# Kernel tuning notes

Measured on AMD Instinct MI355X. Metric: run time of the kernel, lower is better.

Reference implementation:

```python
import jax, jax.numpy as jnp
import numpy as np

T, B, F = 512, 512, 14
H1, H2 = 32, 64


def setup_inputs() -> dict:
    key = jax.random.key(0)
    ks = jax.random.split(key, 16)
    s1 = 1.0 / np.sqrt(H1)
    s2 = 1.0 / np.sqrt(H2)
    u = lambda k, shape, s: jax.random.uniform(k, shape, jnp.float32, -s, s)
    return {
        "x": jax.random.normal(ks[0], (T, B, F), jnp.float32),
        # LSTM layer 1 (PyTorch gate order i,f,g,o)
        "W_ih1": u(ks[1], (4 * H1, F), s1),
        "W_hh1": u(ks[2], (4 * H1, H1), s1),
        "b_ih1": u(ks[3], (4 * H1,), s1),
        "b_hh1": u(ks[4], (4 * H1,), s1),
        # LSTM layer 2
        "W_ih2": u(ks[5], (4 * H2, H1), s2),
        "W_hh2": u(ks[6], (4 * H2, H2), s2),
        "b_ih2": u(ks[7], (4 * H2,), s2),
        "b_hh2": u(ks[8], (4 * H2,), s2),
        # MLP head
        "W_fc1": u(ks[9], (8, H2), 1.0 / np.sqrt(H2)),
        "b_fc1": u(ks[10], (8,), 1.0 / np.sqrt(H2)),
        "W_fc2": u(ks[11], (8, 8), 1.0 / np.sqrt(8)),
        "b_fc2": u(ks[12], (8,), 1.0 / np.sqrt(8)),
        "W_fc": u(ks[13], (1, 8), 1.0 / np.sqrt(8)),
        "b_fc": u(ks[14], (1,), 1.0 / np.sqrt(8)),
    }


def _gates(g, c):
    # PyTorch LSTM gate order: input, forget, cell(g), output
    i, f, gg, o = jnp.split(g, 4, axis=-1)
    c_new = jax.nn.sigmoid(f) * c + jax.nn.sigmoid(i) * jnp.tanh(gg)
    h_new = jax.nn.sigmoid(o) * jnp.tanh(c_new)
    return h_new, c_new


def reference(x, W_ih1, W_hh1, b_ih1, b_hh1, W_ih2, W_hh2, b_ih2, b_hh2,
              W_fc1, b_fc1, W_fc2, b_fc2, W_fc, b_fc):
    Bv = x.shape[1]
    # Fold the input projection of layer 1 outside the scan (one big GEMM).
    xg = jnp.einsum('tbf,gf->tbg', x, W_ih1) + b_ih1 + b_hh1  # [T,B,4H1]

    def step(carry, xg_t):
        h1, c1, h2 = carry
        h1, c1 = _gates(xg_t + h1 @ W_hh1.T, c1)
        # Layer 2: original code never carries c_t2 -> incoming cell is always 0.
        g2 = h1 @ W_ih2.T + b_ih2 + h2 @ W_hh2.T + b_hh2
        h2, _ = _gates(g2, jnp.zeros((Bv, H2), x.dtype))
        return (h1, c1, h2), None

    init = (jnp.zeros((Bv, H1), x.dtype),
            jnp.zeros((Bv, H1), x.dtype),
            jnp.zeros((Bv, H2), x.dtype))
    (h1, c1, h2), _ = jax.lax.scan(step, init, xg)

    out = jax.nn.relu(h2)
    out = jax.nn.relu(out @ W_fc1.T + b_fc1)
    out = jax.nn.relu(out @ W_fc2.T + b_fc2)
    return out @ W_fc.T + b_fc  # [B,1]
```

## Files before the change

kernel.cpp:

```cpp
#include <hip/hip_runtime.h>
#include <math.h>

#define TT 512
#define BB 512
#define FF 14
#define H1 32
#define H2 64
#define NR 8
#define NBLK (BB / NR)

typedef _Float16 half8   __attribute__((ext_vector_type(8)));
typedef _Float16 half4_t __attribute__((ext_vector_type(4)));
typedef float    float4v __attribute__((ext_vector_type(4)));

typedef __attribute__((address_space(1))) const half4_t g_half4;

#if __has_builtin(__builtin_amdgcn_exp2f)
__device__ __forceinline__ float exp2_(float x) { return __builtin_amdgcn_exp2f(x); }
#else
__device__ __forceinline__ float exp2_(float x) { return exp2f(x); }
#endif
__device__ __forceinline__ float rcpf_(float x) { return __builtin_amdgcn_rcpf(x); }

__device__ __forceinline__ float dpp_ror8_(float v) {
    return __int_as_float(__builtin_amdgcn_update_dpp(
        0, __float_as_int(v), 0x128 , 0xF, 0xF, true));
}

#define K1L 1.4426950408889634f
#define K2L 2.8853901617779268f

__device__ __forceinline__ float4v mfma16(half8 a, half8 b, float4v c) {
    return __builtin_amdgcn_mfma_f32_16x16x32_f16(a, b, c, 0, 0, 0);
}

__device__ __forceinline__ int bfrag_off(int k, int n) {
    const int slab = k >> 5, k5 = k & 31;
    const int dl = n + 16 * ((k5 >> 3) & 3);
    const int dw = (k5 >> 1) & 3;
    return ((slab * 256 + dl * 4 + dw) << 1) | (k5 & 1);
}

__global__ __launch_bounds__(512)
void xg_precompute(const float* __restrict__ x,
                   const float* __restrict__ Wih1,
                   const float* __restrict__ bih1,
                   const float* __restrict__ bhh1,
                   _Float16* __restrict__ xg)
{
    const int t    = blockIdx.x >> 3;
    const int seg  = blockIdx.x & 7;
    const int l    = threadIdx.x;
    const int lane = l & 63;
    const int w    = l >> 6;
    const int n    = lane & 15;
    const int quad = lane >> 4;
    const int u1   = w * 4 + quad;

    __shared__ __align__(16) float xs[64 * FF];

    {
        const float* src = x + ((size_t)t * BB + seg * 64) * FF;
        if (l < 448) {
            const float2 v = ((const float2*)src)[l];
            ((float2*)xs)[l] = v;
        }
    }

    float wr[4][FF];
    float bs[4];
    #pragma unroll
    for (int r = 0; r < 4; ++r) {
        const int row = r * 32 + u1;
        #pragma unroll
        for (int f = 0; f < FF; ++f) wr[r][f] = Wih1[row * FF + f];
        bs[r] = bih1[row] + bhh1[row];
    }
    __syncthreads();

    half4_t* og = (half4_t*)xg + (size_t)t * (NBLK * 256);
    #pragma unroll 2
    for (int bi = 0; bi < 8; ++bi) {
        const int blk = seg * 8 + bi;
        const int rb  = (bi * 8 + (n & 7)) * FF;
        float xv[FF];
        #pragma unroll
        for (int e = 0; e < 7; ++e) {
            const float2 v = *(const float2*)&xs[rb + 2 * e];
            xv[2 * e] = v.x; xv[2 * e + 1] = v.y;
        }
        half4_t o16;
        #pragma unroll
        for (int r = 0; r < 4; ++r) {
            float a = bs[r];
            #pragma unroll
            for (int f = 0; f < FF; ++f) a = fmaf(xv[f], wr[r][f], a);
            o16[r] = (_Float16)a;
        }
        if (n < 8) og[blk * 256 + u1 * 8 + n] = o16;
    }
}

#define XGOFF(t_) ((size_t)(t_) * (NBLK * 256))

__global__ __launch_bounds__(768)
__attribute__((amdgpu_waves_per_eu(3, 3)))
void lstm3_v23(
    const _Float16* __restrict__ xg,
    const float* __restrict__ Wih2, const float* __restrict__ Whh1,
    const float* __restrict__ Whh2,
    const float* __restrict__ bih2, const float* __restrict__ bhh2,
    const float* __restrict__ Wfc1, const float* __restrict__ bfc1,
    const float* __restrict__ Wfc2, const float* __restrict__ bfc2,
    const float* __restrict__ Wfc,  const float* __restrict__ bfc,
    float* __restrict__ out)
{
    const int row0 = blockIdx.x * NR;
    const int l    = threadIdx.x;
    const int lane = l & 63;
    const int wv   = l >> 6;
    const bool isL1 = (wv < 4);
    const int w2   = wv - 4;
    const int n    = lane & 15;
    const int quad = lane >> 4;
    const int hi   = n >> 3;

    __shared__ __align__(16) unsigned s2f[2][3 * 256];
    __shared__ _Float16 h2plain[NR][H2];
    __shared__ float mlp1[NR][8];
    __shared__ float mlp2[NR][8];

    half8 a2[2][3];
    float4v bias2[2];
    if (!isL1) {
        #pragma unroll
        for (int tt = 0; tt < 2; ++tt) {
            const int T = 2 * w2 + tt;
            const int m = T * 16 + n;
            const int row = (m & 3) * 64 + (m >> 2);
            #pragma unroll
            for (int s = 0; s < 3; ++s) {
                const int k0 = s * 32 + quad * 8;
                half8 a;
                if (k0 < H1) {
                    #pragma unroll
                    for (int j = 0; j < 8; ++j) a[j] = (_Float16)Wih2[row * H1 + k0 + j];
                } else {
                    #pragma unroll
                    for (int j = 0; j < 8; ++j) a[j] = (_Float16)Whh2[row * H2 + (k0 - H1) + j];
                }
                a2[tt][s] = a;
            }
            const int u = T * 4 + quad;
            #pragma unroll
            for (int r = 0; r < 4; ++r) {
                const int br = r * 64 + u;
                bias2[tt][r] = bih2[br] + bhh2[br];
            }
        }
    }

    half8 a1h0, a1h1;
    if (isL1) {
        #pragma unroll
        for (int tt = 0; tt < 2; ++tt) {
            const int m = (2 * wv + tt) * 16 + n;
            const int row = (m & 3) * 32 + (m >> 2);
            half8 a;
            #pragma unroll
            for (int j = 0; j < 8; ++j)
                a[j] = (_Float16)Whh1[row * H1 + quad * 8 + j];
            if (tt == 0) a1h0 = a; else a1h1 = a;
        }
    }

    const int u1sel = (2 * wv + hi) * 4 + quad;
    const int offB  = bfrag_off(u1sel & 31, n & 7);
    const int u2sel = (2 * w2 + hi) * 4 + quad;
    const int off2n = bfrag_off(32 + (u2sel & 63), n & 7);

    const g_half4* xgb = (const g_half4*)((const half4_t*)xg
                        + (size_t)blockIdx.x * 256 + ((u1sel & 31) * 8 + (n & 7)));

    float c1r = 0.0f;

    for (int z = l; z < 2 * 3 * 256; z += 768) ((unsigned*)s2f)[z] = 0u;

    half4_t xg0 = {0,0,0,0}, xgA = {0,0,0,0}, xgB = {0,0,0,0},
            xgC = {0,0,0,0}, xgD = {0,0,0,0};
    if (isL1) {
        xg0 = xgb[XGOFF(0)];
        xgA = xgb[XGOFF(1)];
        xgB = xgb[XGOFF(2)];
        xgC = xgb[XGOFF(3)];
        xgD = xgb[XGOFF(4)];
    }
    __syncthreads();

#define LSTM_STEP(i_, CP_, RP_, XG_) do {                                          \
        if (isL1) {                                                                \
            const half8 tb0 = *(const half8*)(s2f[RP_] + lane * 4);                \
            const half4_t xh = XG_;                                                \
            { int tn_ = (i_) + 4; if (tn_ > TT - 1) tn_ = TT - 1;                  \
              XG_ = xgb[XGOFF(tn_)]; }                                             \
            const float4v z4 = {0.0f, 0.0f, 0.0f, 0.0f};                           \
            float4v p0 = mfma16(a1h0, tb0, z4);                                    \
            float4v p1 = mfma16(a1h1, tb0, z4);                                    \
            float4v ps;                                                            \
            _Pragma("unroll")                                                      \
            for (int r = 0; r < 4; ++r) {                                          \
                const float sw = dpp_ror8_(p1[r]);                                 \
                ps[r] = hi ? sw : p0[r];                                           \
            }                                                                      \
            const float g0 = ps[0] + (float)xh[0];                                 \
            const float g1 = ps[1] + (float)xh[1];                                 \
            const float g2 = ps[2] + (float)xh[2];                                 \
            const float g3 = ps[3] + (float)xh[3];                                 \
            const float Ei = exp2_(-K1L * g0);                                     \
            const float Ef = exp2_(-K1L * g1);                                     \
            const float Eg = exp2_(-K2L * g2);                                     \
            const float Eo = exp2_(-K1L * g3);                                     \
            const float P  = (1.0f + Ei) * (1.0f + Eg);                            \
            const float pf = 1.0f + Ef;                                            \
            const float cn = fmaf(c1r, P, pf * (1.0f - Eg)) * rcpf_(pf * P);       \
            c1r = cn;                                                              \
            const float Ec = exp2_(-K2L * cn);                                     \
            const float hh = (1.0f - Ec) * rcpf_((1.0f + Eo) * (1.0f + Ec));       \
            ((_Float16*)s2f[CP_])[offB] = (_Float16)hh;                            \
        } else {                                                                   \
            const half8 tb0 = *(const half8*)(s2f[RP_] + lane * 4);                \
            const half8 tb1 = *(const half8*)(s2f[RP_] + 256 + lane * 4);          \
            const half8 tb2 = *(const half8*)(s2f[RP_] + 512 + lane * 4);          \
            float4v p0 = bias2[0];                                                 \
            p0 = mfma16(a2[0][0], tb0, p0);                                        \
            p0 = mfma16(a2[0][1], tb1, p0);                                        \
            p0 = mfma16(a2[0][2], tb2, p0);                                        \
            float4v p1 = bias2[1];                                                 \
            p1 = mfma16(a2[1][0], tb0, p1);                                        \
            p1 = mfma16(a2[1][1], tb1, p1);                                        \
            p1 = mfma16(a2[1][2], tb2, p1);                                        \
            float4v ps;                                                            \
            _Pragma("unroll")                                                      \
            for (int r = 0; r < 4; ++r) {                                          \
                const float sw = dpp_ror8_(p1[r]);                                 \
                ps[r] = hi ? sw : p0[r];                                           \
            }                                                                      \
            const float Ei = exp2_(-K1L * ps[0]);                                  \
            const float Eg = exp2_(-K2L * ps[2]);                                  \
            const float Eo = exp2_(-K1L * ps[3]);                                  \
            const float c2 = (1.0f - Eg) * rcpf_((1.0f + Ei) * (1.0f + Eg));       \
            const float Ec = exp2_(-K2L * c2);                                     \
            const float h  = (1.0f - Ec) * rcpf_((1.0f + Eo) * (1.0f + Ec));       \
            ((_Float16*)s2f[CP_])[off2n] = (_Float16)h;                            \
        }                                                                          \
        asm volatile("s_waitcnt lgkmcnt(0)" ::: "memory");                         \
        __builtin_amdgcn_s_barrier();                                              \
        asm volatile("" ::: "memory");                                             \
    } while (0)

    {
        if (isL1) {
            const float gi = (float)xg0[0], gg = (float)xg0[2], go = (float)xg0[3];
            const float Ei = exp2_(-K1L * gi);
            const float Eg = exp2_(-K2L * gg);
            const float Eo = exp2_(-K1L * go);
            const float cn = (1.0f - Eg) * rcpf_((1.0f + Ei) * (1.0f + Eg));
            c1r = cn;
            const float Ec = exp2_(-K2L * cn);
            const float hh = (1.0f - Ec) * rcpf_((1.0f + Eo) * (1.0f + Ec));
            ((_Float16*)s2f[0])[offB] = (_Float16)hh;
        }
        asm volatile("s_waitcnt lgkmcnt(0)" ::: "memory");
        __builtin_amdgcn_s_barrier();
        asm volatile("" ::: "memory");
    }

    #pragma unroll 1
    for (int ii = 0; ii < 127; ++ii) {
        const int i0 = 4 * ii + 1;
        LSTM_STEP(i0,     1, 0, xgA);
        LSTM_STEP(i0 + 1, 0, 1, xgB);
        LSTM_STEP(i0 + 2, 1, 0, xgC);
        LSTM_STEP(i0 + 3, 0, 1, xgD);
    }
    LSTM_STEP(509, 1, 0, xgA);
    LSTM_STEP(510, 0, 1, xgB);
    LSTM_STEP(511, 1, 0, xgC);

    if (!isL1) {
        const half8 tb0 = *(const half8*)(s2f[1] + lane * 4);
        const half8 tb1 = *(const half8*)(s2f[1] + 256 + lane * 4);
        const half8 tb2 = *(const half8*)(s2f[1] + 512 + lane * 4);
        float4v p0 = bias2[0];
        p0 = mfma16(a2[0][0], tb0, p0);
        p0 = mfma16(a2[0][1], tb1, p0);
        p0 = mfma16(a2[0][2], tb2, p0);
        float4v p1 = bias2[1];
        p1 = mfma16(a2[1][0], tb0, p1);
        p1 = mfma16(a2[1][1], tb1, p1);
        p1 = mfma16(a2[1][2], tb2, p1);
        float4v ps;
        #pragma unroll
        for (int r = 0; r < 4; ++r) {
            const float sw = dpp_ror8_(p1[r]);
            ps[r] = hi ? sw : p0[r];
        }
        const float Ei = exp2_(-K1L * ps[0]);
        const float Eg = exp2_(-K2L * ps[2]);
        const float Eo = exp2_(-K1L * ps[3]);
        const float c2 = (1.0f - Eg) * rcpf_((1.0f + Ei) * (1.0f + Eg));
        const float Ec = exp2_(-K2L * c2);
        const float h  = (1.0f - Ec) * rcpf_((1.0f + Eo) * (1.0f + Ec));
        h2plain[n & 7][u2sel] = (_Float16)h;
    }
    __syncthreads();

    if (l < NR * 8) {
        const int rr = l >> 3, j = l & 7;
        float a = bfc1[j];
        #pragma unroll
        for (int k = 0; k < H2; ++k)
            a = fmaf(fmaxf((float)h2plain[rr][k], 0.0f), Wfc1[j * H2 + k], a);
        mlp1[rr][j] = fmaxf(a, 0.0f);
    }
    __syncthreads();
    if (l < NR * 8) {
        const int rr = l >> 3, j = l & 7;
        float a = bfc2[j];
        #pragma unroll
        for (int k = 0; k < 8; ++k) a = fmaf(mlp1[rr][k], Wfc2[j * 8 + k], a);
        mlp2[rr][j] = fmaxf(a, 0.0f);
    }
    __syncthreads();
    if (l < NR) {
        float a = bfc[0];
        #pragma unroll
        for (int k = 0; k < 8; ++k) a = fmaf(mlp2[l][k], Wfc[k], a);
        out[row0 + l] = a;
    }
#undef LSTM_STEP
}

__device__ __forceinline__ float sigmoidf_(float x) { return rcpf_(1.0f + __expf(-x)); }
__device__ __forceinline__ float tanhf_(float x) {
    float e = __expf(-2.0f * fabsf(x));
    float t = (1.0f - e) * rcpf_(1.0f + e);
    return copysignf(t, x);
}

__global__ __launch_bounds__(512)
__attribute__((amdgpu_waves_per_eu(2, 2)))
void lstm3_kernel(
    const float* __restrict__ x,
    const float* __restrict__ Wih1, const float* __restrict__ Whh1,
    const float* __restrict__ bih1, const float* __restrict__ bhh1,
    const float* __restrict__ Wih2, const float* __restrict__ Whh2,
    const float* __restrict__ bih2, const float* __restrict__ bhh2,
    const float* __restrict__ Wfc1, const float* __restrict__ bfc1,
    const float* __restrict__ Wfc2, const float* __restrict__ bfc2,
    const float* __restrict__ Wfc,  const float* __restrict__ bfc,
    float* __restrict__ out)
{
    const int row0 = blockIdx.x * 16;
    const int l    = threadIdx.x;
    const int lane = l & 63;
    const int w    = l >> 6;
    const int n    = lane & 15;
    const int quad = lane >> 4;

    __shared__ __align__(16) unsigned s2f[2][3 * 256];
    __shared__ _Float16 h2plain[16][H2];
    __shared__ float mlp1[16][8];
    __shared__ float mlp2[16][8];

    half8 a2[2][3];
    float4v bias2[2];
    #pragma unroll
    for (int tt = 0; tt < 2; ++tt) {
        const int T = 2 * w + tt;
        const int m = T * 16 + n;
        const int row = (m & 3) * 64 + (m >> 2);
        #pragma unroll
        for (int s = 0; s < 3; ++s) {
            const int k0 = s * 32 + quad * 8;
            half8 a;
            if (k0 < H1) {
                #pragma unroll
                for (int j = 0; j < 8; ++j) a[j] = (_Float16)Wih2[row * H1 + k0 + j];
            } else {
                #pragma unroll
                for (int j = 0; j < 8; ++j) a[j] = (_Float16)Whh2[row * H2 + (k0 - H1) + j];
            }
            a2[tt][s] = a;
        }
        const int u = T * 4 + quad;
        #pragma unroll
        for (int r = 0; r < 4; ++r) {
            const int br = r * 64 + u;
            bias2[tt][r] = bih2[br] + bhh2[br];
        }
    }

    half8 a1x, a1h;
    float4v bias1;
    {
        const int m = w * 16 + n;
        const int row = (m & 3) * 32 + (m >> 2);
        #pragma unroll
        for (int j = 0; j < 8; ++j) {
            const int k = quad * 8 + j;
            a1x[j] = (_Float16)((k < FF) ? Wih1[row * FF + k] : 0.0f);
            a1h[j] = (_Float16)Whh1[row * H1 + k];
        }
        const int u1_ = w * 4 + quad;
        #pragma unroll
        for (int r = 0; r < 4; ++r) {
            const int br = r * 32 + u1_;
            bias1[r] = bih1[br] + bhh1[br];
        }
    }

    const int u1   = w * 4 + quad;
    const int offB = bfrag_off(u1, n);
    int off2[2];
    #pragma unroll
    for (int tt = 0; tt < 2; ++tt)
        off2[tt] = bfrag_off(32 + (2 * w + tt) * 4 + quad, n);

    const int b1q  = quad & 1;
    const int xrow = (row0 + n) * FF;
    const int xo0 = 8 * b1q;
    const int xo1 = 8 * b1q + 2;
    const int xo2 = 8 * b1q + 4;
    const int xo3 = 6 * b1q + 6;

    float c1r = 0.0f;
    float2 xr0[4], xr1[4];

    for (int z = l; z < 2 * 3 * 256; z += 512) ((unsigned*)s2f)[z] = 0u;

    {
        const float* xp = x + xrow;
        xr0[0] = *(const float2*)(xp + xo0);
        xr0[1] = *(const float2*)(xp + xo1);
        xr0[2] = *(const float2*)(xp + xo2);
        xr0[3] = *(const float2*)(xp + xo3);
        const float* xq = x + BB * FF + xrow;
        xr1[0] = *(const float2*)(xq + xo0);
        xr1[1] = *(const float2*)(xq + xo1);
        xr1[2] = *(const float2*)(xq + xo2);
        xr1[3] = *(const float2*)(xq + xo3);
    }
    __syncthreads();

#define LSTM_STEP_F(i_, CP_, RP_, XR_) do {                                        \
        const half8 tb0 = *(const half8*)(s2f[RP_] + lane * 4);                    \
        const half8 tb1 = *(const half8*)(s2f[RP_] + 256 + lane * 4);              \
        const half8 tb2 = *(const half8*)(s2f[RP_] + 512 + lane * 4);              \
        half8 xb;                                                                  \
        xb[0] = (_Float16)XR_[0].x; xb[1] = (_Float16)XR_[0].y;                    \
        xb[2] = (_Float16)XR_[1].x; xb[3] = (_Float16)XR_[1].y;                    \
        xb[4] = (_Float16)XR_[2].x; xb[5] = (_Float16)XR_[2].y;                    \
        xb[6] = (_Float16)XR_[3].x; xb[7] = (_Float16)XR_[3].y;                    \
        { int tn_ = (i_) + 2; if (tn_ > TT - 1) tn_ = TT - 1;                      \
          const float* xp_ = x + tn_ * (BB * FF) + xrow;                           \
          XR_[0] = *(const float2*)(xp_ + xo0);                                    \
          XR_[1] = *(const float2*)(xp_ + xo1);                                    \
          XR_[2] = *(const float2*)(xp_ + xo2);                                    \
          XR_[3] = *(const float2*)(xp_ + xo3); }                                  \
        float4v acc1 = mfma16(a1x, xb, bias1);                                     \
        acc1 = mfma16(a1h, tb0, acc1);                                             \
        const float cn1 = sigmoidf_(acc1[1]) * c1r                                 \
                        + sigmoidf_(acc1[0]) * tanhf_(acc1[2]);                    \
        c1r = cn1;                                                                 \
        ((_Float16*)s2f[CP_])[offB] = (_Float16)(sigmoidf_(acc1[3]) * tanhf_(cn1));\
        _Pragma("unroll")                                                          \
        for (int tt = 0; tt < 2; ++tt) {                                           \
            float4v acc = bias2[tt];                                               \
            acc = mfma16(a2[tt][0], tb0, acc);                                     \
            acc = mfma16(a2[tt][1], tb1, acc);                                     \
            acc = mfma16(a2[tt][2], tb2, acc);                                     \
            const float cn = sigmoidf_(acc[0]) * tanhf_(acc[2]);                   \
            const float h  = sigmoidf_(acc[3]) * tanhf_(cn);                       \
            ((_Float16*)s2f[CP_])[off2[tt]] = (_Float16)h;                         \
        }                                                                          \
        asm volatile("s_waitcnt lgkmcnt(0)" ::: "memory");                         \
        __builtin_amdgcn_s_barrier();                                              \
        asm volatile("" ::: "memory");                                             \
    } while (0)

    {
        half8 xb;
        xb[0] = (_Float16)xr0[0].x; xb[1] = (_Float16)xr0[0].y;
        xb[2] = (_Float16)xr0[1].x; xb[3] = (_Float16)xr0[1].y;
        xb[4] = (_Float16)xr0[2].x; xb[5] = (_Float16)xr0[2].y;
        xb[6] = (_Float16)xr0[3].x; xb[7] = (_Float16)xr0[3].y;
        {   const float* xp_ = x + 2 * (BB * FF) + xrow;
            xr0[0] = *(const float2*)(xp_ + xo0);
            xr0[1] = *(const float2*)(xp_ + xo1);
            xr0[2] = *(const float2*)(xp_ + xo2);
            xr0[3] = *(const float2*)(xp_ + xo3); }
        float4v acc1 = mfma16(a1x, xb, bias1);
        const float cn1 = sigmoidf_(acc1[0]) * tanhf_(acc1[2]);
        c1r = cn1;
        ((_Float16*)s2f[0])[offB] = (_Float16)(sigmoidf_(acc1[3]) * tanhf_(cn1));
        asm volatile("s_waitcnt lgkmcnt(0)" ::: "memory");
        __builtin_amdgcn_s_barrier();
        asm volatile("" ::: "memory");
    }

    #pragma unroll 1
    for (int ii = 0; ii < 255; ++ii) {
        const int i0 = 2 * ii + 1;
        LSTM_STEP_F(i0,     1, 0, xr1);
        LSTM_STEP_F(i0 + 1, 0, 1, xr0);
    }
    LSTM_STEP_F(511, 1, 0, xr1);

    {
        const half8 tb0 = *(const half8*)(s2f[1] + lane * 4);
        const half8 tb1 = *(const half8*)(s2f[1] + 256 + lane * 4);
        const half8 tb2 = *(const half8*)(s2f[1] + 512 + lane * 4);
        #pragma unroll
        for (int tt = 0; tt < 2; ++tt) {
            float4v acc = bias2[tt];
            acc = mfma16(a2[tt][0], tb0, acc);
            acc = mfma16(a2[tt][1], tb1, acc);
            acc = mfma16(a2[tt][2], tb2, acc);
            const float cn = sigmoidf_(acc[0]) * tanhf_(acc[2]);
            const float h  = sigmoidf_(acc[3]) * tanhf_(cn);
            h2plain[n][(2 * w + tt) * 4 + quad] = (_Float16)h;
        }
        __syncthreads();
    }

    if (l < 16 * 8) {
        const int rr = l >> 3, j = l & 7;
        float a = bfc1[j];
        #pragma unroll
        for (int k = 0; k < H2; ++k)
            a = fmaf(fmaxf((float)h2plain[rr][k], 0.0f), Wfc1[j * H2 + k], a);
        mlp1[rr][j] = fmaxf(a, 0.0f);
    }
    __syncthreads();
    if (l < 16 * 8) {
        const int rr = l >> 3, j = l & 7;
        float a = bfc2[j];
        #pragma unroll
        for (int k = 0; k < 8; ++k) a = fmaf(mlp1[rr][k], Wfc2[j * 8 + k], a);
        mlp2[rr][j] = fmaxf(a, 0.0f);
    }
    __syncthreads();
    if (l < 16) {
        float a = bfc[0];
        #pragma unroll
        for (int k = 0; k < 8; ++k) a = fmaf(mlp2[l][k], Wfc[k], a);
        out[row0 + l] = a;
    }
#undef LSTM_STEP_F
}

extern "C" void kernel_launch(void* const* d_in, const int* in_sizes, int n_in,
                              void* d_out, int out_size, void* d_ws, size_t ws_size,
                              hipStream_t stream) {
    const float* x    = (const float*)d_in[0];
    const float* Wih1 = (const float*)d_in[1];
    const float* Whh1 = (const float*)d_in[2];
    const float* bih1 = (const float*)d_in[3];
    const float* bhh1 = (const float*)d_in[4];
    const float* Wih2 = (const float*)d_in[5];
    const float* Whh2 = (const float*)d_in[6];
    const float* bih2 = (const float*)d_in[7];
    const float* bhh2 = (const float*)d_in[8];
    const float* Wfc1 = (const float*)d_in[9];
    const float* bfc1 = (const float*)d_in[10];
    const float* Wfc2 = (const float*)d_in[11];
    const float* bfc2 = (const float*)d_in[12];
    const float* Wfc  = (const float*)d_in[13];
    const float* bfc  = (const float*)d_in[14];
    float* out = (float*)d_out;

    const size_t xg_bytes = (size_t)TT * NBLK * 256 * sizeof(half4_t);
    if (d_ws != nullptr && ws_size >= xg_bytes) {
        _Float16* xg = (_Float16*)d_ws;
        xg_precompute<<<dim3(TT * 8), dim3(512), 0, stream>>>(x, Wih1, bih1, bhh1, xg);
        lstm3_v23<<<dim3(NBLK), dim3(768), 0, stream>>>(
            xg, Wih2, Whh1, Whh2, bih2, bhh2,
            Wfc1, bfc1, Wfc2, bfc2, Wfc, bfc, out);
    } else {
        lstm3_kernel<<<dim3(BB / 16), dim3(512), 0, stream>>>(
            x, Wih1, Whh1, bih1, bhh1, Wih2, Whh2, bih2, bhh2,
            Wfc1, bfc1, Wfc2, bfc2, Wfc, bfc, out);
    }
}
```

Before: 297.8 us.

## Halve batch rows per block and widen per-wave MFMA tiles in LSTM recurrence

Each block of the recurrent kernel now handles 4 batch rows instead of 8, which doubles the block count to 128. Each block runs 6 waves instead of 12, and each wave computes four MFMA gate tiles instead of two. The tile results are combined with three DPP row rotations and a 4-way select. The xg layout keeps 64 super-blocks, and each block indexes its half through blockIdx parity. The aim is to spread the latency-bound recurrence over more CUs with fewer waves per block, at the cost of more MFMAs per wave on the serial critical path and MFMA columns that are only half used.

```diff
diff --git a/kernel.cpp b/kernel.cpp
--- a/kernel.cpp
+++ b/kernel.cpp
@@ -6,8 +6,9 @@
 #define FF 14
 #define H1 32
 #define H2 64
-#define NR 8
+#define NR 4
 #define NBLK (BB / NR)
+#define XSB 64
 
 typedef _Float16 half8   __attribute__((ext_vector_type(8)));
 typedef _Float16 half4_t __attribute__((ext_vector_type(4)));
@@ -22,9 +23,17 @@
 #endif
 __device__ __forceinline__ float rcpf_(float x) { return __builtin_amdgcn_rcpf(x); }
 
+__device__ __forceinline__ float dpp_ror4_(float v) {
+    return __int_as_float(__builtin_amdgcn_update_dpp(
+        0, __float_as_int(v), 0x124, 0xF, 0xF, true));
+}
 __device__ __forceinline__ float dpp_ror8_(float v) {
     return __int_as_float(__builtin_amdgcn_update_dpp(
-        0, __float_as_int(v), 0x128 , 0xF, 0xF, true));
+        0, __float_as_int(v), 0x128, 0xF, 0xF, true));
+}
+__device__ __forceinline__ float dpp_ror12_(float v) {
+    return __int_as_float(__builtin_amdgcn_update_dpp(
+        0, __float_as_int(v), 0x12C, 0xF, 0xF, true));
 }
 
 #define K1L 1.4426950408889634f
@@ -78,10 +87,10 @@
     }
     __syncthreads();
 
-    half4_t* og = (half4_t*)xg + (size_t)t * (NBLK * 256);
+    half4_t* og = (half4_t*)xg + (size_t)t * (XSB * 256);
     #pragma unroll 2
     for (int bi = 0; bi < 8; ++bi) {
-        const int blk = seg * 8 + bi;
+        const int sb  = seg * 8 + bi;
         const int rb  = (bi * 8 + (n & 7)) * FF;
         float xv[FF];
         #pragma unroll
@@ -97,15 +106,15 @@
             for (int f = 0; f < FF; ++f) a = fmaf(xv[f], wr[r][f], a);
             o16[r] = (_Float16)a;
         }
-        if (n < 8) og[blk * 256 + u1 * 8 + n] = o16;
-    }
-}
-
-#define XGOFF(t_) ((size_t)(t_) * (NBLK * 256))
-
-__global__ __launch_bounds__(768)
-__attribute__((amdgpu_waves_per_eu(3, 3)))
-void lstm3_v23(
+        if (n < 8) og[sb * 256 + u1 * 8 + n] = o16;
+    }
+}
+
+#define XGOFF(t_) ((size_t)(t_) * (XSB * 256))
+
+__global__ __launch_bounds__(384)
+__attribute__((amdgpu_waves_per_eu(2, 2)))
+void lstm3_v24(
     const _Float16* __restrict__ xg,
     const float* __restrict__ Wih2, const float* __restrict__ Whh1,
     const float* __restrict__ Whh2,
@@ -119,23 +128,24 @@
     const int l    = threadIdx.x;
     const int lane = l & 63;
     const int wv   = l >> 6;
-    const bool isL1 = (wv < 4);
-    const int w2   = wv - 4;
+    const bool isL1 = (wv < 2);
+    const int w2   = wv - 2;
     const int n    = lane & 15;
     const int quad = lane >> 4;
-    const int hi   = n >> 3;
+    const int sq   = n >> 2;
+    const int cc   = n & 3;
 
     __shared__ __align__(16) unsigned s2f[2][3 * 256];
     __shared__ _Float16 h2plain[NR][H2];
     __shared__ float mlp1[NR][8];
     __shared__ float mlp2[NR][8];
 
-    half8 a2[2][3];
-    float4v bias2[2];
+    half8 a2[4][3];
+    float4v bias2[4];
     if (!isL1) {
         #pragma unroll
-        for (int tt = 0; tt < 2; ++tt) {
-            const int T = 2 * w2 + tt;
+        for (int tt = 0; tt < 4; ++tt) {
+            const int T = 4 * w2 + tt;
             const int m = T * 16 + n;
             const int row = (m & 3) * 64 + (m >> 2);
             #pragma unroll
@@ -160,31 +170,35 @@
         }
     }
 
-    half8 a1h0, a1h1;
+    half8 a1h0, a1h1, a1h2, a1h3;
     if (isL1) {
         #pragma unroll
-        for (int tt = 0; tt < 2; ++tt) {
-            const int m = (2 * wv + tt) * 16 + n;
+        for (int tt = 0; tt < 4; ++tt) {
+            const int m = (4 * wv + tt) * 16 + n;
             const int row = (m & 3) * 32 + (m >> 2);
             half8 a;
             #pragma unroll
             for (int j = 0; j < 8; ++j)
                 a[j] = (_Float16)Whh1[row * H1 + quad * 8 + j];
-            if (tt == 0) a1h0 = a; else a1h1 = a;
-        }
-    }
-
-    const int u1sel = (2 * wv + hi) * 4 + quad;
-    const int offB  = bfrag_off(u1sel & 31, n & 7);
-    const int u2sel = (2 * w2 + hi) * 4 + quad;
-    const int off2n = bfrag_off(32 + (u2sel & 63), n & 7);
+            if      (tt == 0) a1h0 = a;
+            else if (tt == 1) a1h1 = a;
+            else if (tt == 2) a1h2 = a;
+            else              a1h3 = a;
+        }
+    }
+
+    const int u1sel = (4 * wv + sq) * 4 + quad;
+    const int offB  = bfrag_off(u1sel & 31, cc);
+    const int u2sel = (4 * w2 + sq) * 4 + quad;
+    const int off2n = bfrag_off(32 + (u2sel & 63), cc);
 
     const g_half4* xgb = (const g_half4*)((const half4_t*)xg
-                        + (size_t)blockIdx.x * 256 + ((u1sel & 31) * 8 + (n & 7)));
+            + (size_t)(blockIdx.x >> 1) * 256
+            + ((u1sel & 31) * 8 + (blockIdx.x & 1) * 4 + cc));
 
     float c1r = 0.0f;
 
-    for (int z = l; z < 2 * 3 * 256; z += 768) ((unsigned*)s2f)[z] = 0u;
+    for (int z = l; z < 2 * 3 * 256; z += 384) ((unsigned*)s2f)[z] = 0u;
 
     half4_t xg0 = {0,0,0,0}, xgA = {0,0,0,0}, xgB = {0,0,0,0},
             xgC = {0,0,0,0}, xgD = {0,0,0,0};
@@ -196,6 +210,18 @@
         xgD = xgb[XGOFF(4)];
     }
     __syncthreads();
+
+#define MERGE4(PS_, P0_, P1_, P2_, P3_) do {                                       \
+        _Pragma("unroll")                                                          \
+        for (int r = 0; r < 4; ++r) {                                              \
+            const float q1 = dpp_ror12_(P1_[r]);                                   \
+            const float q2 = dpp_ror8_(P2_[r]);                                    \
+            const float q3 = dpp_ror4_(P3_[r]);                                    \
+            const float t01 = (sq == 1) ? q1 : P0_[r];                             \
+            const float t23 = (sq == 3) ? q3 : q2;                                 \
+            PS_[r] = (sq >= 2) ? t23 : t01;                                        \
+        }                                                                          \
+    } while (0)
 
 #define LSTM_STEP(i_, CP_, RP_, XG_) do {                                          \
         if (isL1) {                                                                \
@@ -206,12 +232,10 @@
             const float4v z4 = {0.0f, 0.0f, 0.0f, 0.0f};                           \
             float4v p0 = mfma16(a1h0, tb0, z4);                                    \
             float4v p1 = mfma16(a1h1, tb0, z4);                                    \
+            float4v p2 = mfma16(a1h2, tb0, z4);                                    \
+            float4v p3 = mfma16(a1h3, tb0, z4);                                    \
             float4v ps;                                                            \
-            _Pragma("unroll")                                                      \
-            for (int r = 0; r < 4; ++r) {                                          \
-                const float sw = dpp_ror8_(p1[r]);                                 \
-                ps[r] = hi ? sw : p0[r];                                           \
-            }                                                                      \
+            MERGE4(ps, p0, p1, p2, p3);                                            \
             const float g0 = ps[0] + (float)xh[0];                                 \
             const float g1 = ps[1] + (float)xh[1];                                 \
             const float g2 = ps[2] + (float)xh[2];                                 \
@@ -239,12 +263,16 @@
             p1 = mfma16(a2[1][0], tb0, p1);                                        \
             p1 = mfma16(a2[1][1], tb1, p1);                                        \
             p1 = mfma16(a2[1][2], tb2, p1);                                        \
+            float4v p2 = bias2[2];                                                 \
+            p2 = mfma16(a2[2][0], tb0, p2);                                        \
+            p2 = mfma16(a2[2][1], tb1, p2);                                        \
+            p2 = mfma16(a2[2][2], tb2, p2);                                        \
+            float4v p3 = bias2[3];                                                 \
+            p3 = mfma16(a2[3][0], tb0, p3);                                        \
+            p3 = mfma16(a2[3][1], tb1, p3);                                        \
+            p3 = mfma16(a2[3][2], tb2, p3);                                        \
             float4v ps;                                                            \
-            _Pragma("unroll")                                                      \
-            for (int r = 0; r < 4; ++r) {                                          \
-                const float sw = dpp_ror8_(p1[r]);                                 \
-                ps[r] = hi ? sw : p0[r];                                           \
-            }                                                                      \
+            MERGE4(ps, p0, p1, p2, p3);                                            \
             const float Ei = exp2_(-K1L * ps[0]);                                  \
             const float Eg = exp2_(-K2L * ps[2]);                                  \
             const float Eo = exp2_(-K1L * ps[3]);                                  \
@@ -299,19 +327,23 @@
         p1 = mfma16(a2[1][0], tb0, p1);
         p1 = mfma16(a2[1][1], tb1, p1);
         p1 = mfma16(a2[1][2], tb2, p1);
+        float4v p2 = bias2[2];
+        p2 = mfma16(a2[2][0], tb0, p2);
+        p2 = mfma16(a2[2][1], tb1, p2);
+        p2 = mfma16(a2[2][2], tb2, p2);
+        float4v p3 = bias2[3];
+        p3 = mfma16(a2[3][0], tb0, p3);
+        p3 = mfma16(a2[3][1], tb1, p3);
+        p3 = mfma16(a2[3][2], tb2, p3);
         float4v ps;
-        #pragma unroll
-        for (int r = 0; r < 4; ++r) {
-            const float sw = dpp_ror8_(p1[r]);
-            ps[r] = hi ? sw : p0[r];
-        }
+        MERGE4(ps, p0, p1, p2, p3);
         const float Ei = exp2_(-K1L * ps[0]);
         const float Eg = exp2_(-K2L * ps[2]);
         const float Eo = exp2_(-K1L * ps[3]);
         const float c2 = (1.0f - Eg) * rcpf_((1.0f + Ei) * (1.0f + Eg));
         const float Ec = exp2_(-K2L * c2);
         const float h  = (1.0f - Ec) * rcpf_((1.0f + Eo) * (1.0f + Ec));
-        h2plain[n & 7][u2sel] = (_Float16)h;
+        h2plain[cc][u2sel] = (_Float16)h;
     }
     __syncthreads();
 
@@ -339,6 +371,7 @@
         out[row0 + l] = a;
     }
 #undef LSTM_STEP
+#undef MERGE4
 }
 
 __device__ __forceinline__ float sigmoidf_(float x) { return rcpf_(1.0f + __expf(-x)); }
@@ -580,11 +613,11 @@
     const float* bfc  = (const float*)d_in[14];
     float* out = (float*)d_out;
 
-    const size_t xg_bytes = (size_t)TT * NBLK * 256 * sizeof(half4_t);
+    const size_t xg_bytes = (size_t)TT * XSB * 256 * sizeof(half4_t);
     if (d_ws != nullptr && ws_size >= xg_bytes) {
         _Float16* xg = (_Float16*)d_ws;
         xg_precompute<<<dim3(TT * 8), dim3(512), 0, stream>>>(x, Wih1, bih1, bhh1, xg);
-        lstm3_v23<<<dim3(NBLK), dim3(768), 0, stream>>>(
+        lstm3_v24<<<dim3(NBLK), dim3(384), 0, stream>>>(
             xg, Wih2, Whh1, Whh2, bih2, bhh2,
             Wfc1, bfc1, Wfc2, bfc2, Wfc, bfc, out);
     } else {
```

Measured after the change: 298.1 us. About the same (+0.1%).

## Interleave two independent 8-row batch groups per LSTM block

Applied to the files above, without the earlier changes.

Each recurrent block now carries two independent 8-row batch groups, A and B. Each group has its own shared-memory h buffers, cell-state registers and xg prefetch registers. The MFMA and activation work of the two groups is interleaved inside every time step, so the two dependency chains can hide each other's latency. This halves the grid to 32 blocks and lengthens each step's instruction stream, and it shares one barrier per step between both groups. The xg workspace is re-indexed by 8-row sub-block so the precompute kernel stays unchanged.

```diff
diff --git a/kernel.cpp b/kernel.cpp
--- a/kernel.cpp
+++ b/kernel.cpp
@@ -6,8 +6,10 @@
 #define FF 14
 #define H1 32
 #define H2 64
-#define NR 8
+#define NRG 8
+#define NR 16
 #define NBLK (BB / NR)
+#define XSB 64
 
 typedef _Float16 half8   __attribute__((ext_vector_type(8)));
 typedef _Float16 half4_t __attribute__((ext_vector_type(4)));
@@ -78,10 +80,10 @@
     }
     __syncthreads();
 
-    half4_t* og = (half4_t*)xg + (size_t)t * (NBLK * 256);
+    half4_t* og = (half4_t*)xg + (size_t)t * (XSB * 256);
     #pragma unroll 2
     for (int bi = 0; bi < 8; ++bi) {
-        const int blk = seg * 8 + bi;
+        const int sb  = seg * 8 + bi;
         const int rb  = (bi * 8 + (n & 7)) * FF;
         float xv[FF];
         #pragma unroll
@@ -97,15 +99,15 @@
             for (int f = 0; f < FF; ++f) a = fmaf(xv[f], wr[r][f], a);
             o16[r] = (_Float16)a;
         }
-        if (n < 8) og[blk * 256 + u1 * 8 + n] = o16;
-    }
-}
-
-#define XGOFF(t_) ((size_t)(t_) * (NBLK * 256))
+        if (n < 8) og[sb * 256 + u1 * 8 + n] = o16;
+    }
+}
+
+#define XGOFF(t_) ((size_t)(t_) * (XSB * 256))
 
 __global__ __launch_bounds__(768)
 __attribute__((amdgpu_waves_per_eu(3, 3)))
-void lstm3_v23(
+void lstm3_v26(
     const _Float16* __restrict__ xg,
     const float* __restrict__ Wih2, const float* __restrict__ Whh1,
     const float* __restrict__ Whh2,
@@ -125,7 +127,8 @@
     const int quad = lane >> 4;
     const int hi   = n >> 3;
 
-    __shared__ __align__(16) unsigned s2f[2][3 * 256];
+    __shared__ __align__(16) unsigned s2fA[2][3 * 256];
+    __shared__ __align__(16) unsigned s2fB[2][3 * 256];
     __shared__ _Float16 h2plain[NR][H2];
     __shared__ float mlp1[NR][8];
     __shared__ float mlp2[NR][8];
@@ -179,79 +182,108 @@
     const int u2sel = (2 * w2 + hi) * 4 + quad;
     const int off2n = bfrag_off(32 + (u2sel & 63), n & 7);
 
-    const g_half4* xgb = (const g_half4*)((const half4_t*)xg
-                        + (size_t)blockIdx.x * 256 + ((u1sel & 31) * 8 + (n & 7)));
-
-    float c1r = 0.0f;
-
-    for (int z = l; z < 2 * 3 * 256; z += 768) ((unsigned*)s2f)[z] = 0u;
-
-    half4_t xg0 = {0,0,0,0}, xgA = {0,0,0,0}, xgB = {0,0,0,0},
-            xgC = {0,0,0,0}, xgD = {0,0,0,0};
+    const int xge = (u1sel & 31) * 8 + (n & 7);
+    const g_half4* xgbA = (const g_half4*)((const half4_t*)xg
+                        + (size_t)(2 * blockIdx.x)     * 256 + xge);
+    const g_half4* xgbB = (const g_half4*)((const half4_t*)xg
+                        + (size_t)(2 * blockIdx.x + 1) * 256 + xge);
+
+    float c1rA = 0.0f, c1rB = 0.0f;
+
+    for (int z = l; z < 2 * 3 * 256; z += 768) {
+        ((unsigned*)s2fA)[z] = 0u;
+        ((unsigned*)s2fB)[z] = 0u;
+    }
+
+    half4_t xg0A = {0,0,0,0}, rA1 = {0,0,0,0}, rA2 = {0,0,0,0},
+            rA3 = {0,0,0,0}, rA4 = {0,0,0,0};
+    half4_t xg0B = {0,0,0,0}, rB1 = {0,0,0,0}, rB2 = {0,0,0,0},
+            rB3 = {0,0,0,0}, rB4 = {0,0,0,0};
     if (isL1) {
-        xg0 = xgb[XGOFF(0)];
-        xgA = xgb[XGOFF(1)];
-        xgB = xgb[XGOFF(2)];
-        xgC = xgb[XGOFF(3)];
-        xgD = xgb[XGOFF(4)];
-    }
-    __syncthreads();
-
-#define LSTM_STEP(i_, CP_, RP_, XG_) do {                                          \
+        xg0A = xgbA[XGOFF(0)];  xg0B = xgbB[XGOFF(0)];
+        rA1 = xgbA[XGOFF(1)];   rB1 = xgbB[XGOFF(1)];
+        rA2 = xgbA[XGOFF(2)];   rB2 = xgbB[XGOFF(2)];
+        rA3 = xgbA[XGOFF(3)];   rB3 = xgbB[XGOFF(3)];
+        rA4 = xgbA[XGOFF(4)];   rB4 = xgbB[XGOFF(4)];
+    }
+    __syncthreads();
+
+#define L1ACT(SF_, CP_, PS_, XH_, C1_) do {                                        \
+        const float g0 = PS_[0] + (float)XH_[0];                                   \
+        const float g1 = PS_[1] + (float)XH_[1];                                   \
+        const float g2 = PS_[2] + (float)XH_[2];                                   \
+        const float g3 = PS_[3] + (float)XH_[3];                                   \
+        const float Ei = exp2_(-K1L * g0);                                         \
+        const float Ef = exp2_(-K1L * g1);                                         \
+        const float Eg = exp2_(-K2L * g2);                                         \
+        const float Eo = exp2_(-K1L * g3);                                         \
+        const float P  = (1.0f + Ei) * (1.0f + Eg);                                \
+        const float pf = 1.0f + Ef;                                                \
+        const float cn = fmaf(C1_, P, pf * (1.0f - Eg)) * rcpf_(pf * P);           \
+        C1_ = cn;                                                                  \
+        const float Ec = exp2_(-K2L * cn);                                         \
+        const float hh = (1.0f - Ec) * rcpf_((1.0f + Eo) * (1.0f + Ec));           \
+        ((_Float16*)SF_[CP_])[offB] = (_Float16)hh;                                \
+    } while (0)
+
+#define L2ACT(SF_, CP_, PS_) do {                                                  \
+        const float Ei = exp2_(-K1L * PS_[0]);                                     \
+        const float Eg = exp2_(-K2L * PS_[2]);                                     \
+        const float Eo = exp2_(-K1L * PS_[3]);                                     \
+        const float c2 = (1.0f - Eg) * rcpf_((1.0f + Ei) * (1.0f + Eg));           \
+        const float Ec = exp2_(-K2L * c2);                                         \
+        const float h  = (1.0f - Ec) * rcpf_((1.0f + Eo) * (1.0f + Ec));           \
+        ((_Float16*)SF_[CP_])[off2n] = (_Float16)h;                                \
+    } while (0)
+
+#define LSTM_STEP(i_, CP_, RP_, XGA_, XGB_) do {                                   \
         if (isL1) {                                                                \
-            const half8 tb0 = *(const half8*)(s2f[RP_] + lane * 4);                \
-            const half4_t xh = XG_;                                                \
+            const half8 tbA = *(const half8*)(s2fA[RP_] + lane * 4);               \
+            const half8 tbB = *(const half8*)(s2fB[RP_] + lane * 4);               \
+            const half4_t xhA = XGA_;                                              \
+            const half4_t xhB = XGB_;                                              \
             { int tn_ = (i_) + 4; if (tn_ > TT - 1) tn_ = TT - 1;                  \
-              XG_ = xgb[XGOFF(tn_)]; }                                             \
+              XGA_ = xgbA[XGOFF(tn_)]; XGB_ = xgbB[XGOFF(tn_)]; }                  \
             const float4v z4 = {0.0f, 0.0f, 0.0f, 0.0f};                           \
-            float4v p0 = mfma16(a1h0, tb0, z4);                                    \
-            float4v p1 = mfma16(a1h1, tb0, z4);                                    \
-            float4v ps;                                                            \
+            float4v pA0 = mfma16(a1h0, tbA, z4);                                   \
+            float4v pB0 = mfma16(a1h0, tbB, z4);                                   \
+            float4v pA1 = mfma16(a1h1, tbA, z4);                                   \
+            float4v pB1 = mfma16(a1h1, tbB, z4);                                   \
+            float4v psA, psB;                                                      \
             _Pragma("unroll")                                                      \
             for (int r = 0; r < 4; ++r) {                                          \
-                const float sw = dpp_ror8_(p1[r]);                                 \
-                ps[r] = hi ? sw : p0[r];                                           \
+                const float swA = dpp_ror8_(pA1[r]);                               \
+                const float swB = dpp_ror8_(pB1[r]);                               \
+                psA[r] = hi ? swA : pA0[r];                                        \
+                psB[r] = hi ? swB : pB0[r];                                        \
             }                                                                      \
-            const float g0 = ps[0] + (float)xh[0];                                 \
-            const float g1 = ps[1] + (float)xh[1];                                 \
-            const float g2 = ps[2] + (float)xh[2];                                 \
-            const float g3 = ps[3] + (float)xh[3];                                 \
-            const float Ei = exp2_(-K1L * g0);                                     \
-            const float Ef = exp2_(-K1L * g1);                                     \
-            const float Eg = exp2_(-K2L * g2);                                     \
-            const float Eo = exp2_(-K1L * g3);                                     \
-            const float P  = (1.0f + Ei) * (1.0f + Eg);                            \
-            const float pf = 1.0f + Ef;                                            \
-            const float cn = fmaf(c1r, P, pf * (1.0f - Eg)) * rcpf_(pf * P);       \
-            c1r = cn;                                                              \
-            const float Ec = exp2_(-K2L * cn);                                     \
-            const float hh = (1.0f - Ec) * rcpf_((1.0f + Eo) * (1.0f + Ec));       \
-            ((_Float16*)s2f[CP_])[offB] = (_Float16)hh;                            \
+            L1ACT(s2fA, CP_, psA, xhA, c1rA);                                      \
+            L1ACT(s2fB, CP_, psB, xhB, c1rB);                                      \
         } else {                                                                   \
-            const half8 tb0 = *(const half8*)(s2f[RP_] + lane * 4);                \
-            const half8 tb1 = *(const half8*)(s2f[RP_] + 256 + lane * 4);          \
-            const half8 tb2 = *(const half8*)(s2f[RP_] + 512 + lane * 4);          \
-            float4v p0 = bias2[0];                                                 \
-            p0 = mfma16(a2[0][0], tb0, p0);                                        \
-            p0 = mfma16(a2[0][1], tb1, p0);                                        \
-            p0 = mfma16(a2[0][2], tb2, p0);                                        \
-            float4v p1 = bias2[1];                                                 \
-            p1 = mfma16(a2[1][0], tb0, p1);                                        \
-            p1 = mfma16(a2[1][1], tb1, p1);                                        \
-            p1 = mfma16(a2[1][2], tb2, p1);                                        \
-            float4v ps;                                                            \
+            const half8 tA0 = *(const half8*)(s2fA[RP_] + lane * 4);               \
+            const half8 tA1 = *(const half8*)(s2fA[RP_] + 256 + lane * 4);         \
+            const half8 tA2 = *(const half8*)(s2fA[RP_] + 512 + lane * 4);         \
+            const half8 tB0 = *(const half8*)(s2fB[RP_] + lane * 4);               \
+            const half8 tB1 = *(const half8*)(s2fB[RP_] + 256 + lane * 4);         \
+            const half8 tB2 = *(const half8*)(s2fB[RP_] + 512 + lane * 4);         \
+            float4v pA0 = bias2[0], pA1 = bias2[1];                                \
+            float4v pB0 = bias2[0], pB1 = bias2[1];                                \
+            pA0 = mfma16(a2[0][0], tA0, pA0); pB0 = mfma16(a2[0][0], tB0, pB0);    \
+            pA1 = mfma16(a2[1][0], tA0, pA1); pB1 = mfma16(a2[1][0], tB0, pB1);    \
+            pA0 = mfma16(a2[0][1], tA1, pA0); pB0 = mfma16(a2[0][1], tB1, pB0);    \
+            pA1 = mfma16(a2[1][1], tA1, pA1); pB1 = mfma16(a2[1][1], tB1, pB1);    \
+            pA0 = mfma16(a2[0][2], tA2, pA0); pB0 = mfma16(a2[0][2], tB2, pB0);    \
+            pA1 = mfma16(a2[1][2], tA2, pA1); pB1 = mfma16(a2[1][2], tB2, pB1);    \
+            float4v psA, psB;                                                      \
             _Pragma("unroll")                                                      \
             for (int r = 0; r < 4; ++r) {                                          \
-                const float sw = dpp_ror8_(p1[r]);                                 \
-                ps[r] = hi ? sw : p0[r];                                           \
+                const float swA = dpp_ror8_(pA1[r]);                               \
+                const float swB = dpp_ror8_(pB1[r]);                               \
+                psA[r] = hi ? swA : pA0[r];                                        \
+                psB[r] = hi ? swB : pB0[r];                                        \
             }                                                                      \
-            const float Ei = exp2_(-K1L * ps[0]);                                  \
-            const float Eg = exp2_(-K2L * ps[2]);                                  \
-            const float Eo = exp2_(-K1L * ps[3]);                                  \
-            const float c2 = (1.0f - Eg) * rcpf_((1.0f + Ei) * (1.0f + Eg));       \
-            const float Ec = exp2_(-K2L * c2);                                     \
-            const float h  = (1.0f - Ec) * rcpf_((1.0f + Eo) * (1.0f + Ec));       \
-            ((_Float16*)s2f[CP_])[off2n] = (_Float16)h;                            \
+            L2ACT(s2fA, CP_, psA);                                                 \
+            L2ACT(s2fB, CP_, psB);                                                 \
         }                                                                          \
         asm volatile("s_waitcnt lgkmcnt(0)" ::: "memory");                         \
         __builtin_amdgcn_s_barrier();                                              \
@@ -260,15 +292,28 @@
 
     {
         if (isL1) {
-            const float gi = (float)xg0[0], gg = (float)xg0[2], go = (float)xg0[3];
-            const float Ei = exp2_(-K1L * gi);
-            const float Eg = exp2_(-K2L * gg);
-            const float Eo = exp2_(-K1L * go);
-            const float cn = (1.0f - Eg) * rcpf_((1.0f + Ei) * (1.0f + Eg));
-            c1r = cn;
-            const float Ec = exp2_(-K2L * cn);
-            const float hh = (1.0f - Ec) * rcpf_((1.0f + Eo) * (1.0f + Ec));
-            ((_Float16*)s2f[0])[offB] = (_Float16)hh;
+            {
+                const float gi = (float)xg0A[0], gg = (float)xg0A[2], go = (float)xg0A[3];
+                const float Ei = exp2_(-K1L * gi);
+                const float Eg = exp2_(-K2L * gg);
+                const float Eo = exp2_(-K1L * go);
+                const float cn = (1.0f - Eg) * rcpf_((1.0f + Ei) * (1.0f + Eg));
+                c1rA = cn;
+                const float Ec = exp2_(-K2L * cn);
+                const float hh = (1.0f - Ec) * rcpf_((1.0f + Eo) * (1.0f + Ec));
+                ((_Float16*)s2fA[0])[offB] = (_Float16)hh;
+            }
+            {
+                const float gi = (float)xg0B[0], gg = (float)xg0B[2], go = (float)xg0B[3];
+                const float Ei = exp2_(-K1L * gi);
+                const float Eg = exp2_(-K2L * gg);
+                const float Eo = exp2_(-K1L * go);
+                const float cn = (1.0f - Eg) * rcpf_((1.0f + Ei) * (1.0f + Eg));
+                c1rB = cn;
+                const float Ec = exp2_(-K2L * cn);
+                const float hh = (1.0f - Ec) * rcpf_((1.0f + Eo) * (1.0f + Ec));
+                ((_Float16*)s2fB[0])[offB] = (_Float16)hh;
+            }
         }
         asm volatile("s_waitcnt lgkmcnt(0)" ::: "memory");
         __builtin_amdgcn_s_barrier();
@@ -278,40 +323,56 @@
     #pragma unroll 1
     for (int ii = 0; ii < 127; ++ii) {
         const int i0 = 4 * ii + 1;
-        LSTM_STEP(i0,     1, 0, xgA);
-        LSTM_STEP(i0 + 1, 0, 1, xgB);
-        LSTM_STEP(i0 + 2, 1, 0, xgC);
-        LSTM_STEP(i0 + 3, 0, 1, xgD);
-    }
-    LSTM_STEP(509, 1, 0, xgA);
-    LSTM_STEP(510, 0, 1, xgB);
-    LSTM_STEP(511, 1, 0, xgC);
+        LSTM_STEP(i0,     1, 0, rA1, rB1);
+        LSTM_STEP(i0 + 1, 0, 1, rA2, rB2);
+        LSTM_STEP(i0 + 2, 1, 0, rA3, rB3);
+        LSTM_STEP(i0 + 3, 0, 1, rA4, rB4);
+    }
+    LSTM_STEP(509, 1, 0, rA1, rB1);
+    LSTM_STEP(510, 0, 1, rA2, rB2);
+    LSTM_STEP(511, 1, 0, rA3, rB3);
 
     if (!isL1) {
-        const half8 tb0 = *(const half8*)(s2f[1] + lane * 4);
-        const half8 tb1 = *(const half8*)(s2f[1] + 256 + lane * 4);
-        const half8 tb2 = *(const half8*)(s2f[1] + 512 + lane * 4);
-        float4v p0 = bias2[0];
-        p0 = mfma16(a2[0][0], tb0, p0);
-        p0 = mfma16(a2[0][1], tb1, p0);
-        p0 = mfma16(a2[0][2], tb2, p0);
-        float4v p1 = bias2[1];
-        p1 = mfma16(a2[1][0], tb0, p1);
-        p1 = mfma16(a2[1][1], tb1, p1);
-        p1 = mfma16(a2[1][2], tb2, p1);
-        float4v ps;
+        const half8 tA0 = *(const half8*)(s2fA[1] + lane * 4);
+        const half8 tA1 = *(const half8*)(s2fA[1] + 256 + lane * 4);
+        const half8 tA2 = *(const half8*)(s2fA[1] + 512 + lane * 4);
+        const half8 tB0 = *(const half8*)(s2fB[1] + lane * 4);
+        const half8 tB1 = *(const half8*)(s2fB[1] + 256 + lane * 4);
+        const half8 tB2 = *(const half8*)(s2fB[1] + 512 + lane * 4);
+        float4v pA0 = bias2[0], pA1 = bias2[1];
+        float4v pB0 = bias2[0], pB1 = bias2[1];
+        pA0 = mfma16(a2[0][0], tA0, pA0); pB0 = mfma16(a2[0][0], tB0, pB0);
+        pA1 = mfma16(a2[1][0], tA0, pA1); pB1 = mfma16(a2[1][0], tB0, pB1);
+        pA0 = mfma16(a2[0][1], tA1, pA0); pB0 = mfma16(a2[0][1], tB1, pB0);
+        pA1 = mfma16(a2[1][1], tA1, pA1); pB1 = mfma16(a2[1][1], tB1, pB1);
+        pA0 = mfma16(a2[0][2], tA2, pA0); pB0 = mfma16(a2[0][2], tB2, pB0);
+        pA1 = mfma16(a2[1][2], tA2, pA1); pB1 = mfma16(a2[1][2], tB2, pB1);
+        float4v psA, psB;
         #pragma unroll
         for (int r = 0; r < 4; ++r) {
-            const float sw = dpp_ror8_(p1[r]);
-            ps[r] = hi ? sw : p0[r];
-        }
-        const float Ei = exp2_(-K1L * ps[0]);
-        const float Eg = exp2_(-K2L * ps[2]);
-        const float Eo = exp2_(-K1L * ps[3]);
-        const float c2 = (1.0f - Eg) * rcpf_((1.0f + Ei) * (1.0f + Eg));
-        const float Ec = exp2_(-K2L * c2);
-        const float h  = (1.0f - Ec) * rcpf_((1.0f + Eo) * (1.0f + Ec));
-        h2plain[n & 7][u2sel] = (_Float16)h;
+            const float swA = dpp_ror8_(pA1[r]);
+            const float swB = dpp_ror8_(pB1[r]);
+            psA[r] = hi ? swA : pA0[r];
+            psB[r] = hi ? swB : pB0[r];
+        }
+        {
+            const float Ei = exp2_(-K1L * psA[0]);
+            const float Eg = exp2_(-K2L * psA[2]);
+            const float Eo = exp2_(-K1L * psA[3]);
+            const float c2 = (1.0f - Eg) * rcpf_((1.0f + Ei) * (1.0f + Eg));
+            const float Ec = exp2_(-K2L * c2);
+            const float h  = (1.0f - Ec) * rcpf_((1.0f + Eo) * (1.0f + Ec));
+            h2plain[n & 7][u2sel] = (_Float16)h;
+        }
+        {
+            const float Ei = exp2_(-K1L * psB[0]);
+            const float Eg = exp2_(-K2L * psB[2]);
+            const float Eo = exp2_(-K1L * psB[3]);
+            const float c2 = (1.0f - Eg) * rcpf_((1.0f + Ei) * (1.0f + Eg));
+            const float Ec = exp2_(-K2L * c2);
+            const float h  = (1.0f - Ec) * rcpf_((1.0f + Eo) * (1.0f + Ec));
+            h2plain[8 + (n & 7)][u2sel] = (_Float16)h;
+        }
     }
     __syncthreads();
 
@@ -339,6 +400,8 @@
         out[row0 + l] = a;
     }
 #undef LSTM_STEP
+#undef L1ACT
+#undef L2ACT
 }
 
 __device__ __forceinline__ float sigmoidf_(float x) { return rcpf_(1.0f + __expf(-x)); }
@@ -580,11 +643,11 @@
     const float* bfc  = (const float*)d_in[14];
     float* out = (float*)d_out;
 
-    const size_t xg_bytes = (size_t)TT * NBLK * 256 * sizeof(half4_t);
+    const size_t xg_bytes = (size_t)TT * XSB * 256 * sizeof(half4_t);
     if (d_ws != nullptr && ws_size >= xg_bytes) {
         _Float16* xg = (_Float16*)d_ws;
         xg_precompute<<<dim3(TT * 8), dim3(512), 0, stream>>>(x, Wih1, bih1, bhh1, xg);
-        lstm3_v23<<<dim3(NBLK), dim3(768), 0, stream>>>(
+        lstm3_v26<<<dim3(NBLK), dim3(768), 0, stream>>>(
             xg, Wih2, Whh1, Whh2, bih2, bhh2,
             Wfc1, bfc1, Wfc2, bfc2, Wfc, bfc, out);
     } else {
```

Measured after the change: 412.1 us. 38.4% more time.
